# Kernel tuning notes

Hardware: AMD Instinct MI355X
Metric: run time of the kernel (lower is better)

Reference implementation:

```python
import jax, jax.numpy as jnp
import numpy as np
import math

B, SQ, SK, D_MODEL, OUT_DIM = 8, 2048, 2048, 1024, 128
MASK_VALUE = -1e6  # torch code fills masked scores with -1000000.0, not -inf


def setup_inputs() -> dict:
    key = jax.random.key(0)
    ks = jax.random.split(key, 10)
    scale = 1.0 / math.sqrt(D_MODEL)
    return {
        "queries": jax.random.normal(ks[0], (B, SQ, D_MODEL), dtype=jnp.float32),
        "keys": jax.random.normal(ks[1], (B, SK, D_MODEL), dtype=jnp.float32),
        "values": jax.random.normal(ks[2], (B, SK, D_MODEL), dtype=jnp.float32),
        "valid_lens": jax.random.randint(ks[3], (B,), 1, SK + 1, dtype=jnp.int32),
        "w_q": jax.random.normal(ks[4], (D_MODEL, OUT_DIM), dtype=jnp.float32) * scale,
        "b_q": jnp.zeros((OUT_DIM,), dtype=jnp.float32),
        "w_k": jax.random.normal(ks[5], (D_MODEL, OUT_DIM), dtype=jnp.float32) * scale,
        "b_k": jnp.zeros((OUT_DIM,), dtype=jnp.float32),
        "w_v": jax.random.normal(ks[6], (D_MODEL, OUT_DIM), dtype=jnp.float32) * scale,
        "b_v": jnp.zeros((OUT_DIM,), dtype=jnp.float32),
    }


def reference(queries, keys, values, valid_lens, w_q, b_q, w_k, b_k, w_v, b_v):
    # QKV projections (LazyLinear equivalents)
    Q = queries @ w_q + b_q   # [B, SQ, OUT_DIM]
    K = keys @ w_k + b_k      # [B, SK, OUT_DIM]
    V = values @ w_v + b_v    # [B, SK, OUT_DIM]
    dim = Q.shape[-1]
    scores = jnp.einsum("bqd,bkd->bqk", Q, K) / jnp.sqrt(jnp.asarray(dim, Q.dtype))
    # masked_softmax: valid_lens [B] -> mask positions >= valid_len on the key axis
    mask = jnp.arange(scores.shape[-1])[None, None, :] < valid_lens[:, None, None]
    scores = jnp.where(mask, scores, jnp.asarray(MASK_VALUE, scores.dtype))
    attn = jax.nn.softmax(scores, axis=-1)
    return jnp.einsum("bqk,bkd->bqd", attn, V)  # [B, SQ, OUT_DIM]
```

## Files before the change

kernel.cpp:

```cpp
#include <hip/hip_runtime.h>
#include <math.h>

constexpr int BATCH  = 8;
constexpr int SEQQ   = 2048;
constexpr int SEQK   = 2048;
constexpr int DMODEL = 1024;
constexpr int ODIM   = 128;

typedef __attribute__((ext_vector_type(8))) short bf16x8;
typedef __attribute__((ext_vector_type(4))) float f32x4;

__device__ inline unsigned short f2bf(float f) {
    union { float f; unsigned int u; } v; v.f = f;
    unsigned int r = v.u + 0x7FFFu + ((v.u >> 16) & 1u);
    return (unsigned short)(r >> 16);
}

__device__ __forceinline__ unsigned int pk2bf(float a, float b) {
    unsigned int ua = __float_as_uint(a) + 0x8000u;
    unsigned int ub = __float_as_uint(b) + 0x8000u;
    return __builtin_amdgcn_perm(ub, ua, 0x07060302u);
}

__device__ __forceinline__ void gl_lds16(const void* g, void* l) {
    __builtin_amdgcn_global_load_lds(
        (const __attribute__((address_space(1))) unsigned int*)g,
        (__attribute__((address_space(3))) unsigned int*)l, 16, 0, 0);
}

__global__ __launch_bounds__(256)
void wtrans_kernel(const float* __restrict__ Wq, const float* __restrict__ Wk,
                   const float* __restrict__ Wv, unsigned short* __restrict__ Wt)
{
    const int which = blockIdx.z;
    const float* __restrict__ W = which == 0 ? Wq : (which == 1 ? Wk : Wv);
    unsigned short* __restrict__ dst = Wt + (size_t)which * DMODEL * ODIM;
    const int k0 = blockIdx.x * 32, n0 = blockIdx.y * 32;
    __shared__ unsigned short T[32][36];
    const int t = threadIdx.x;
    const int r = t >> 3, c = (t & 7) * 4;
    float4 w = *(const float4*)(W + (size_t)(k0 + r) * ODIM + n0 + c);
    T[r][c + 0] = f2bf(w.x); T[r][c + 1] = f2bf(w.y);
    T[r][c + 2] = f2bf(w.z); T[r][c + 3] = f2bf(w.w);
    __syncthreads();
    const int n = t >> 3, k4 = (t & 7) * 4;
    ushort4 o;
    o.x = T[k4 + 0][n]; o.y = T[k4 + 1][n];
    o.z = T[k4 + 2][n]; o.w = T[k4 + 3][n];
    *(ushort4*)(dst + (size_t)(n0 + n) * DMODEL + k0 + k4) = o;
}

#define PSTEP(T, CUR, REGC, REGN, DO_W, DO_A, DO_WR, WSTR, DO_SYNC)           \
  {                                                                            \
    if (DO_W) {                                                                \
      const int kw = ((T) + 1) * 64;                                           \
      _Pragma("unroll")                                                        \
      for (int j = 0; j < 4; ++j)                                              \
        gl_lds16(wgp[j] + kw, &Ws[(CUR) ^ 1][wloff[j]]);                       \
    }                                                                          \
    if (DO_A) {                                                                \
      const int ka = ((T) + 2) * 64;                                           \
      _Pragma("unroll")                                                        \
      for (int j = 0; j < 4; ++j) REGN[j] = *(const float4*)(agp[j] + ka);     \
    }                                                                          \
    _Pragma("unroll")                                                          \
    for (int ks = 0; ks < 2; ++ks) {                                           \
      const int c = (ks * 4 + quad) ^ x;                                       \
      bf16x8 af0 = *(const bf16x8*)&As[CUR][(wrh + lrow) * 64 + c * 8];        \
      bf16x8 af1 = *(const bf16x8*)&As[CUR][(wrh + 16 + lrow) * 64 + c * 8];   \
      _Pragma("unroll")                                                        \
      for (int nt = 0; nt < 4; ++nt) {                                         \
        const int n = wch + nt * 16 + lrow;                                    \
        bf16x8 wf = *(const bf16x8*)&Ws[CUR][n * 64 + c * 8];                  \
        acc[0][nt] = __builtin_amdgcn_mfma_f32_16x16x32_bf16(af0, wf, acc[0][nt], 0, 0, 0); \
        acc[1][nt] = __builtin_amdgcn_mfma_f32_16x16x32_bf16(af1, wf, acc[1][nt], 0, 0, 0); \
      }                                                                        \
    }                                                                          \
    if (DO_WR) {                                                               \
      _Pragma("unroll")                                                        \
      for (int j = 0; j < 4; ++j) {                                            \
        uint2 p;                                                               \
        p.x = pk2bf(REGC[j].x, REGC[j].y);                                     \
        p.y = pk2bf(REGC[j].z, REGC[j].w);                                     \
        *(uint2*)&As[(CUR) ^ 1][awoff[j]] = p;                                 \
      }                                                                        \
    }                                                                          \
    if (DO_SYNC) {                                                             \
      asm volatile("s_waitcnt " WSTR ::: "memory");                            \
      __builtin_amdgcn_sched_barrier(0);                                       \
      __builtin_amdgcn_s_barrier();                                            \
      __builtin_amdgcn_sched_barrier(0);                                       \
    }                                                                          \
  }

__global__ __launch_bounds__(256, 3)
void proj_kernel(const float* __restrict__ Aq, const float* __restrict__ Ak,
                 const float* __restrict__ Av,
                 const unsigned short* __restrict__ Wt_all,
                 const float* __restrict__ bq, const float* __restrict__ bk,
                 const float* __restrict__ bv,
                 unsigned short* __restrict__ Qb, unsigned short* __restrict__ Kb,
                 unsigned short* __restrict__ Vt)
{
    const int which = blockIdx.y;
    const float* __restrict__ A    = which == 0 ? Aq : (which == 1 ? Ak : Av);
    const float* __restrict__ bias = which == 0 ? bq : (which == 1 ? bk : bv);
    const unsigned short* __restrict__ Wt = Wt_all + (size_t)which * DMODEL * ODIM;

    const int row0 = blockIdx.x * 64;
    const int t = threadIdx.x, wave = t >> 6, lane = t & 63;
    const int lrow = lane & 15, quad = lane >> 4;
    const int wrh = (wave & 1) * 32;
    const int wch = (wave >> 1) * 64;

    __shared__ __align__(16) unsigned short As[2][64 * 64];
    __shared__ __align__(16) unsigned short Ws[2][128 * 64];

    f32x4 acc[2][4];
#pragma unroll
    for (int mt = 0; mt < 2; ++mt)
#pragma unroll
        for (int nt = 0; nt < 4; ++nt)
#pragma unroll
            for (int i = 0; i < 4; ++i) acc[mt][nt][i] = 0.f;

    const float* agp[4];
    int awoff[4];
#pragma unroll
    for (int j = 0; j < 4; ++j) {
        const int s = j * 256 + t;
        const int ar = s >> 4, ac = s & 15;
        agp[j]   = A + (size_t)(row0 + ar) * DMODEL + ac * 4;
        awoff[j] = ar * 64 + (((ac >> 1) ^ (ar & 7)) * 8) + (ac & 1) * 4;
    }
    const unsigned short* wgp[4];
    int wloff[4];
#pragma unroll
    for (int j = 0; j < 4; ++j) {
        const int s = j * 256 + t;
        const int wr = s >> 3, wcc = (s & 7) ^ (wr & 7);
        wgp[j]   = Wt + (size_t)wr * DMODEL + wcc * 8;
        wloff[j] = s * 8;
    }

    const int x = lrow & 7;
    float4 ra[4], rb[4];

#pragma unroll
    for (int j = 0; j < 4; ++j) gl_lds16(wgp[j], &Ws[0][wloff[j]]);
#pragma unroll
    for (int j = 0; j < 4; ++j) ra[j] = *(const float4*)(agp[j]);
#pragma unroll
    for (int j = 0; j < 4; ++j) rb[j] = *(const float4*)(agp[j] + 64);
#pragma unroll
    for (int j = 0; j < 4; ++j) {
        uint2 p;
        p.x = pk2bf(ra[j].x, ra[j].y);
        p.y = pk2bf(ra[j].z, ra[j].w);
        *(uint2*)&As[0][awoff[j]] = p;
    }
    asm volatile("s_waitcnt lgkmcnt(0)" ::: "memory");
    __builtin_amdgcn_sched_barrier(0);
    __builtin_amdgcn_s_barrier();
    __builtin_amdgcn_sched_barrier(0);

    for (int kt = 0; kt < 14; kt += 2) {
        PSTEP(kt,     0, rb, ra, 1, 1, 1, "vmcnt(4) lgkmcnt(0)", 1);
        PSTEP(kt + 1, 1, ra, rb, 1, 1, 1, "vmcnt(4) lgkmcnt(0)", 1);
    }
    PSTEP(14, 0, rb, ra, 1, 0, 1, "vmcnt(0) lgkmcnt(0)", 1);
    PSTEP(15, 1, ra, rb, 0, 0, 0, "", 0);

    const float sc = (which == 0) ? 0.08838834764831845f : 1.0f;
    float bv_[4];
#pragma unroll
    for (int nt = 0; nt < 4; ++nt) bv_[nt] = bias[wch + nt * 16 + lrow];

    const int b  = row0 >> 11;
    const int mb = row0 & 2047;

    if (which == 2) {
#pragma unroll
        for (int mt = 0; mt < 2; ++mt)
#pragma unroll
            for (int nt = 0; nt < 4; ++nt) {
                const int n = wch + nt * 16 + lrow;
                ushort4 o;
                o.x = f2bf(acc[mt][nt][0] + bv_[nt]);
                o.y = f2bf(acc[mt][nt][1] + bv_[nt]);
                o.z = f2bf(acc[mt][nt][2] + bv_[nt]);
                o.w = f2bf(acc[mt][nt][3] + bv_[nt]);
                *(ushort4*)(Vt + ((size_t)b * ODIM + n) * SEQK
                            + mb + wrh + mt * 16 + quad * 4) = o;
            }
    } else {
        unsigned short* __restrict__ Ob = (which == 0) ? Qb : Kb;
#pragma unroll
        for (int mt = 0; mt < 2; ++mt)
#pragma unroll
            for (int nt = 0; nt < 4; ++nt)
#pragma unroll
                for (int r = 0; r < 4; ++r) {
                    float val = sc * (acc[mt][nt][r] + bv_[nt]);
                    Ob[(size_t)(row0 + wrh + mt * 16 + quad * 4 + r) * ODIM
                       + wch + nt * 16 + lrow] = f2bf(val);
                }
    }
}

__global__ __launch_bounds__(256, 3)
void flash_kernel(const unsigned short* __restrict__ Qb,
                  const unsigned short* __restrict__ Kb,
                  const unsigned short* __restrict__ Vt,
                  const int* __restrict__ valid_lens,
                  float* __restrict__ Op, float* __restrict__ Lp, int nsplit)
{
    const int b = blockIdx.y, s = blockIdx.z, q0 = blockIdx.x * 64;
    const int skh = SEQK / nsplit;
    const int t = threadIdx.x, wave = t >> 6, lane = t & 63;
    const int lrow = lane & 15, quad = lane >> 4;

    const int valid = valid_lens[b];
    const int vloc  = min(valid - s * skh, skh);

    float* __restrict__ lpart = Lp + (size_t)(s * BATCH + b) * SEQQ + q0;
    float* __restrict__ opart = Op + ((size_t)(s * BATCH + b) * SEQQ + q0) * ODIM;

    if (vloc <= 0) {
        if (t < 64) lpart[t] = 0.f;
        return;
    }

    __shared__ __align__(16) unsigned short Ks[64 * 128];
    __shared__ __align__(16) unsigned short Vs[128 * 64];
    __shared__ __align__(16) unsigned short Ps[4][16][72];

    bf16x8 qf[4];
    {
        const unsigned short* qp =
            Qb + ((size_t)b * SEQQ + q0 + wave * 16 + lrow) * ODIM + quad * 8;
#pragma unroll
        for (int ks = 0; ks < 4; ++ks) qf[ks] = *(const bf16x8*)(qp + ks * 32);
    }

    f32x4 o[8];
#pragma unroll
    for (int nt = 0; nt < 8; ++nt)
#pragma unroll
        for (int i = 0; i < 4; ++i) o[nt][i] = 0.f;
    float lsum[4] = {0.f, 0.f, 0.f, 0.f};

    const unsigned short* kgp[4]; unsigned short* kldst[4];
    const unsigned short* vgp[4]; unsigned short* vldst[4];
    const unsigned short* kbase = Kb + ((size_t)b * SEQK + s * skh) * ODIM;
    const unsigned short* vbase = Vt + (size_t)b * ODIM * SEQK + s * skh;
#pragma unroll
    for (int j = 0; j < 4; ++j) {
        const int sl = j * 256 + t;
        const int kr = sl >> 4, kc = (sl & 15) ^ (kr & 15);
        kgp[j]   = kbase + (size_t)kr * ODIM + kc * 8;
        kldst[j] = &Ks[sl * 8];
        const int vr = sl >> 3, vc = (sl & 7) ^ (vr & 7);
        vgp[j]   = vbase + (size_t)vr * SEQK + vc * 8;
        vldst[j] = &Vs[sl * 8];
    }

    const int x4 = lrow, x3 = lrow & 7;
    const int nch = (vloc + 63) >> 6;

    for (int c = 0; c < nch; ++c) {
        const int k0 = c * 64;
#pragma unroll
        for (int j = 0; j < 4; ++j) {
            gl_lds16(kgp[j] + (size_t)k0 * ODIM, kldst[j]);
            gl_lds16(vgp[j] + k0, vldst[j]);
        }
        __syncthreads();

        f32x4 sv[4];
#pragma unroll
        for (int nt = 0; nt < 4; ++nt)
#pragma unroll
            for (int i = 0; i < 4; ++i) sv[nt][i] = 0.f;
#pragma unroll
        for (int ks = 0; ks < 4; ++ks)
#pragma unroll
            for (int nt = 0; nt < 4; ++nt) {
                const int kr = nt * 16 + lrow;
                const int cc = (ks * 4 + quad) ^ x4;
                bf16x8 kf = *(const bf16x8*)&Ks[(kr * 16 + cc) * 8];
                sv[nt] = __builtin_amdgcn_mfma_f32_16x16x32_bf16(qf[ks], kf, sv[nt], 0, 0, 0);
            }

        if (k0 + 64 > vloc) {
#pragma unroll
            for (int nt = 0; nt < 4; ++nt)
                if (k0 + nt * 16 + lrow >= vloc) {
#pragma unroll
                    for (int i = 0; i < 4; ++i) sv[nt][i] = -1e30f;
                }
        }

#pragma unroll
        for (int nt = 0; nt < 4; ++nt)
#pragma unroll
            for (int r = 0; r < 4; ++r) {
                float p = __expf(sv[nt][r]);
                lsum[r] += p;
                Ps[wave][quad * 4 + r][nt * 16 + lrow] =
                    (unsigned short)((__float_as_uint(p) + 0x8000u) >> 16);
            }

        bf16x8 pf0 = *(const bf16x8*)&Ps[wave][lrow][quad * 8];
        bf16x8 pf1 = *(const bf16x8*)&Ps[wave][lrow][32 + quad * 8];

#pragma unroll
        for (int nt = 0; nt < 8; ++nt) {
            const int vrow = nt * 16 + lrow;
            bf16x8 v0 = *(const bf16x8*)&Vs[(vrow * 8 + (quad ^ x3)) * 8];
            o[nt] = __builtin_amdgcn_mfma_f32_16x16x32_bf16(pf0, v0, o[nt], 0, 0, 0);
        }
#pragma unroll
        for (int nt = 0; nt < 8; ++nt) {
            const int vrow = nt * 16 + lrow;
            bf16x8 v1 = *(const bf16x8*)&Vs[(vrow * 8 + ((4 + quad) ^ x3)) * 8];
            o[nt] = __builtin_amdgcn_mfma_f32_16x16x32_bf16(pf1, v1, o[nt], 0, 0, 0);
        }
        __syncthreads();
    }

#pragma unroll
    for (int msk = 1; msk < 16; msk <<= 1)
#pragma unroll
        for (int r = 0; r < 4; ++r) lsum[r] += __shfl_xor(lsum[r], msk);
    if (lrow == 0) {
#pragma unroll
        for (int r = 0; r < 4; ++r)
            lpart[wave * 16 + quad * 4 + r] = lsum[r];
    }

#pragma unroll
    for (int nt = 0; nt < 8; ++nt)
#pragma unroll
        for (int r = 0; r < 4; ++r)
            opart[(size_t)(wave * 16 + quad * 4 + r) * ODIM + nt * 16 + lrow]
                = o[nt][r];
}

__global__ __launch_bounds__(256)
void combine_kernel(const float* __restrict__ Op, const float* __restrict__ Lp,
                    float* __restrict__ out, int nsplit)
{
    const int idx = blockIdx.x * 256 + threadIdx.x;
    const int row = idx >> 5;
    const size_t SL = (size_t)BATCH * SEQQ;
    float l = 0.f;
    float4 acc = {0.f, 0.f, 0.f, 0.f};
    for (int s = 0; s < nsplit; ++s) {
        float ls = Lp[(size_t)s * SL + row];
        if (ls > 0.f) {
            float4 v = ((const float4*)(Op + (size_t)s * SL * ODIM))[idx];
            acc.x += v.x; acc.y += v.y; acc.z += v.z; acc.w += v.w;
            l += ls;
        }
    }
    const float inv = 1.f / l;
    float4 r;
    r.x = acc.x * inv; r.y = acc.y * inv; r.z = acc.z * inv; r.w = acc.w * inv;
    ((float4*)out)[idx] = r;
}

extern "C" void kernel_launch(void* const* d_in, const int* in_sizes, int n_in,
                              void* d_out, int out_size, void* d_ws, size_t ws_size,
                              hipStream_t stream)
{
    const float* queries    = (const float*)d_in[0];
    const float* keys       = (const float*)d_in[1];
    const float* values     = (const float*)d_in[2];
    const int*   valid_lens = (const int*)d_in[3];
    const float* w_q        = (const float*)d_in[4];
    const float* b_q        = (const float*)d_in[5];
    const float* w_k        = (const float*)d_in[6];
    const float* b_k        = (const float*)d_in[7];
    const float* w_v        = (const float*)d_in[8];
    const float* b_v        = (const float*)d_in[9];
    float* out = (float*)d_out;

    const size_t nQKV = (size_t)BATCH * SEQQ * ODIM;
    unsigned short* Qb = (unsigned short*)d_ws;
    unsigned short* Kb = Qb + nQKV;
    unsigned short* Vt = Kb + nQKV;
    unsigned short* Wt = Vt + nQKV;
    const size_t base = 3 * nQKV * sizeof(unsigned short)
                      + (size_t)3 * DMODEL * ODIM * sizeof(unsigned short);

    int KS = 4;
    if (ws_size < base + 4 * (nQKV * 4 + (size_t)BATCH * SEQQ * 4)) KS = 2;

    float* Op = (float*)((char*)d_ws + base);
    float* Lp = Op + (size_t)KS * nQKV;

    wtrans_kernel<<<dim3(DMODEL / 32, ODIM / 32, 3), 256, 0, stream>>>(w_q, w_k, w_v, Wt);

    proj_kernel<<<dim3((BATCH * SEQQ) / 64, 3), 256, 0, stream>>>(
        queries, keys, values, Wt, b_q, b_k, b_v, Qb, Kb, Vt);

    flash_kernel<<<dim3(SEQQ / 64, BATCH, KS), 256, 0, stream>>>(
        Qb, Kb, Vt, valid_lens, Op, Lp, KS);

    combine_kernel<<<(BATCH * SEQQ * ODIM / 4) / 256, 256, 0, stream>>>(Op, Lp, out, KS);
}
```

Baseline: 246.7 us.

## Double-buffer K/V tiles in flash kernel and lower occupancy hint

Result: slower. 252.6 us (+2.4%).

```diff
diff --git a/kernel.cpp b/kernel.cpp
--- a/kernel.cpp
+++ b/kernel.cpp
@@ -1,5 +1,6 @@
 #include <hip/hip_runtime.h>
 #include <math.h>
+
 
 constexpr int BATCH  = 8;
 constexpr int SEQQ   = 2048;
@@ -93,7 +94,7 @@
     }                                                                          \
   }
 
-__global__ __launch_bounds__(256, 3)
+__global__ __launch_bounds__(256, 2)
 void proj_kernel(const float* __restrict__ Aq, const float* __restrict__ Ak,
                  const float* __restrict__ Av,
                  const unsigned short* __restrict__ Wt_all,
@@ -208,7 +209,7 @@
     }
 }
 
-__global__ __launch_bounds__(256, 3)
+__global__ __launch_bounds__(256, 2)
 void flash_kernel(const unsigned short* __restrict__ Qb,
                   const unsigned short* __restrict__ Kb,
                   const unsigned short* __restrict__ Vt,
@@ -231,8 +232,8 @@
         return;
     }
 
-    __shared__ __align__(16) unsigned short Ks[64 * 128];
-    __shared__ __align__(16) unsigned short Vs[128 * 64];
+    __shared__ __align__(16) unsigned short Ks[2][64 * 128];
+    __shared__ __align__(16) unsigned short Vs[2][128 * 64];
     __shared__ __align__(16) unsigned short Ps[4][16][72];
 
     bf16x8 qf[4];
@@ -250,32 +251,43 @@
         for (int i = 0; i < 4; ++i) o[nt][i] = 0.f;
     float lsum[4] = {0.f, 0.f, 0.f, 0.f};
 
-    const unsigned short* kgp[4]; unsigned short* kldst[4];
-    const unsigned short* vgp[4]; unsigned short* vldst[4];
+    const unsigned short* kgp[4]; int koff[4];
+    const unsigned short* vgp[4]; int voff[4];
     const unsigned short* kbase = Kb + ((size_t)b * SEQK + s * skh) * ODIM;
     const unsigned short* vbase = Vt + (size_t)b * ODIM * SEQK + s * skh;
 #pragma unroll
     for (int j = 0; j < 4; ++j) {
         const int sl = j * 256 + t;
         const int kr = sl >> 4, kc = (sl & 15) ^ (kr & 15);
-        kgp[j]   = kbase + (size_t)kr * ODIM + kc * 8;
-        kldst[j] = &Ks[sl * 8];
+        kgp[j]  = kbase + (size_t)kr * ODIM + kc * 8;
+        koff[j] = sl * 8;
         const int vr = sl >> 3, vc = (sl & 7) ^ (vr & 7);
-        vgp[j]   = vbase + (size_t)vr * SEQK + vc * 8;
-        vldst[j] = &Vs[sl * 8];
+        vgp[j]  = vbase + (size_t)vr * SEQK + vc * 8;
+        voff[j] = sl * 8;
     }
 
     const int x4 = lrow, x3 = lrow & 7;
     const int nch = (vloc + 63) >> 6;
 
+#pragma unroll
+    for (int j = 0; j < 4; ++j) {
+        gl_lds16(kgp[j], &Ks[0][koff[j]]);
+        gl_lds16(vgp[j], &Vs[0][voff[j]]);
+    }
+    __syncthreads();
+
     for (int c = 0; c < nch; ++c) {
-        const int k0 = c * 64;
-#pragma unroll
-        for (int j = 0; j < 4; ++j) {
-            gl_lds16(kgp[j] + (size_t)k0 * ODIM, kldst[j]);
-            gl_lds16(vgp[j] + k0, vldst[j]);
+        const int cur = c & 1;
+        const int k0  = c * 64;
+
+        if (c + 1 < nch) {
+            const int k1 = (c + 1) * 64;
+#pragma unroll
+            for (int j = 0; j < 4; ++j) {
+                gl_lds16(kgp[j] + (size_t)k1 * ODIM, &Ks[cur ^ 1][koff[j]]);
+                gl_lds16(vgp[j] + k1, &Vs[cur ^ 1][voff[j]]);
+            }
         }
-        __syncthreads();
 
         f32x4 sv[4];
 #pragma unroll
@@ -288,7 +300,7 @@
             for (int nt = 0; nt < 4; ++nt) {
                 const int kr = nt * 16 + lrow;
                 const int cc = (ks * 4 + quad) ^ x4;
-                bf16x8 kf = *(const bf16x8*)&Ks[(kr * 16 + cc) * 8];
+                bf16x8 kf = *(const bf16x8*)&Ks[cur][(kr * 16 + cc) * 8];
                 sv[nt] = __builtin_amdgcn_mfma_f32_16x16x32_bf16(qf[ks], kf, sv[nt], 0, 0, 0);
             }
 
@@ -317,13 +329,13 @@
 #pragma unroll
         for (int nt = 0; nt < 8; ++nt) {
             const int vrow = nt * 16 + lrow;
-            bf16x8 v0 = *(const bf16x8*)&Vs[(vrow * 8 + (quad ^ x3)) * 8];
+            bf16x8 v0 = *(const bf16x8*)&Vs[cur][(vrow * 8 + (quad ^ x3)) * 8];
             o[nt] = __builtin_amdgcn_mfma_f32_16x16x32_bf16(pf0, v0, o[nt], 0, 0, 0);
         }
 #pragma unroll
         for (int nt = 0; nt < 8; ++nt) {
             const int vrow = nt * 16 + lrow;
-            bf16x8 v1 = *(const bf16x8*)&Vs[(vrow * 8 + ((4 + quad) ^ x3)) * 8];
+            bf16x8 v1 = *(const bf16x8*)&Vs[cur][(vrow * 8 + ((4 + quad) ^ x3)) * 8];
             o[nt] = __builtin_amdgcn_mfma_f32_16x16x32_bf16(pf1, v1, o[nt], 0, 0, 0);
         }
         __syncthreads();
```
